# Kernel tuning notes

Hardware: AMD Instinct MI355X
Metric: run time of the kernel (lower is better)

## Reference

```python
import jax, jax.numpy as jnp
import numpy as np

B, N, F = 64, 1024, 256  # batch, graph_size, feature dim


def setup_inputs() -> dict:
    key = jax.random.key(0)
    k1, k2, k3, k4, k5 = jax.random.split(key, 5)
    x = jax.random.normal(k1, (B, F), dtype=jnp.float32)
    nodes = jax.random.normal(k2, (B, N, F), dtype=jnp.float32)
    adj = jax.random.uniform(k3, (B, N, N), dtype=jnp.float32)
    # num_nodes in [0, N]; values == N trigger the overflow/wrap path
    num_nodes = jax.random.randint(k4, (B,), 0, N + 1)
    # GNN weight for the dense GCN layer: tanh(adj @ nodes @ W)
    W = jax.random.normal(k5, (F, F), dtype=jnp.float32) * 0.05
    return {"x": x, "nodes": nodes, "adj": adj, "num_nodes": num_nodes, "W": W}


def _wrap_overflow(nodes, adj, num_nodes):
    # FIFO eviction for overflowing batches: zero slot 0 (row/col), roll up by one.
    mask = (num_nodes + 1) > N  # [B]
    w_nodes = jnp.roll(nodes.at[:, 0, :].set(0.0), shift=-1, axis=1)
    w_adj = jnp.roll(adj.at[:, 0, :].set(0.0).at[:, :, 0].set(0.0),
                     shift=(-1, -1), axis=(1, 2))
    nodes = jnp.where(mask[:, None, None], w_nodes, nodes)
    adj = jnp.where(mask[:, None, None], w_adj, adj)
    num_nodes = jnp.where(mask, num_nodes - 1, num_nodes)
    return nodes, adj, num_nodes


def reference(x, nodes, adj, num_nodes, W):
    # 1) wrap-around eviction where the graph is full (masked -> jit friendly;
    #    identical to torch branch since untouched batches are unchanged)
    nodes, adj, num_nodes = _wrap_overflow(nodes, adj, num_nodes)

    # 2) scatter-write new memory x into slot num_nodes[b] of each batch
    b_idx = jnp.arange(B)
    nodes = nodes.at[b_idx, num_nodes].set(x)

    # 3) GNN: dense GCN layer node_feats = tanh((adj @ nodes) @ W)
    node_feats = jnp.tanh(jnp.einsum('bnm,bmf->bnf', adj, nodes) @ W)

    # 4) query: read back the just-written node's embedding (pooled=False)
    mx = node_feats[b_idx, num_nodes]

    return mx, nodes, adj, num_nodes + 1
```

## Files before the change

kernel.cpp:

```cpp
#include <hip/hip_runtime.h>
#include <math.h>

#define B 64
#define N 1024
#define F 256

#define OUT_MX    0
#define OUT_NODES (B * F)
#define OUT_ADJ   (OUT_NODES + B * N * F)
#define OUT_NN    (OUT_ADJ + B * N * N)

__global__ void k_zero(float* __restrict__ t) {
    int i = blockIdx.x * 256 + threadIdx.x;
    if (i < B * F) t[i] = 0.0f;
}

__global__ void k_nodes(const float* __restrict__ x,
                        const float* __restrict__ nodes,
                        const int* __restrict__ num_nodes,
                        float* __restrict__ out) {
    int tid = threadIdx.x;
    int row_in_block = tid >> 6;
    int f4 = (tid & 63) << 2;
    long bi = (long)blockIdx.x * 4 + row_in_block;
    int b = (int)(bi >> 10);
    int i = (int)(bi & (N - 1));
    int nn_in = num_nodes[b];
    bool wrapped = (nn_in == N);
    int nn = wrapped ? (N - 1) : nn_in;
    float4 v;
    if (i == nn) {
        v = *(const float4*)(x + (long)b * F + f4);
    } else {
        long srow = wrapped ? (bi + 1) : bi;
        v = *(const float4*)(nodes + srow * F + f4);
    }
    *(float4*)(out + OUT_NODES + bi * F + f4) = v;
}

__global__ void k_adj(const float* __restrict__ adj,
                      const int* __restrict__ num_nodes,
                      float* __restrict__ out) {
    long bi = blockIdx.x;
    int b = (int)(bi >> 10);
    int i = (int)(bi & (N - 1));
    int j = threadIdx.x << 2;
    bool wrapped = (num_nodes[b] == N);
    float4 v;
    const float* base = adj + (long)b * N * N;
    if (!wrapped) {
        v = *(const float4*)(base + (long)i * N + j);
    } else if (i >= N - 1) {
        v = make_float4(0.f, 0.f, 0.f, 0.f);
    } else {
        const float* r = base + (long)(i + 1) * N;
        v.x = (j + 0 < N - 1) ? r[j + 1] : 0.f;
        v.y = (j + 1 < N - 1) ? r[j + 2] : 0.f;
        v.z = (j + 2 < N - 1) ? r[j + 3] : 0.f;
        v.w = (j + 3 < N - 1) ? r[j + 4] : 0.f;
    }
    *(float4*)(out + OUT_ADJ + bi * N + j) = v;
}

#define MCHUNK 64
__global__ void k_partial(const float* __restrict__ adj,
                          const int* __restrict__ num_nodes,
                          const float* __restrict__ out_nodes,
                          float* __restrict__ t) {
    int b = blockIdx.x >> 4;
    int s = blockIdx.x & 15;
    int nn_in = num_nodes[b];
    if (nn_in == N) return;
    int f = threadIdx.x;
    __shared__ float arow[MCHUNK];
    int m0 = s * MCHUNK;
    if (f < MCHUNK)
        arow[f] = adj[(long)b * N * N + (long)nn_in * N + m0 + f];
    __syncthreads();
    float acc = 0.0f;
    const float* np = out_nodes + ((long)b * N + m0) * F + f;
    #pragma unroll 8
    for (int m = 0; m < MCHUNK; m++)
        acc += arow[m] * np[(long)m * F];
    atomicAdd(&t[b * F + f], acc);
}

__global__ void k_final(const float* __restrict__ t,
                        const float* __restrict__ W,
                        const int* __restrict__ num_nodes,
                        float* __restrict__ out) {
    int b = blockIdx.x;
    int f = threadIdx.x;
    __shared__ float tl[F];
    tl[f] = t[b * F + f];
    __syncthreads();
    float acc = 0.0f;
    #pragma unroll 8
    for (int fp = 0; fp < F; fp++)
        acc += tl[fp] * W[fp * F + f];
    out[OUT_MX + b * F + f] = tanhf(acc);
    if (f == 0) {
        int nn_in = num_nodes[b];
        int nn = (nn_in == N) ? (N - 1) : nn_in;
        out[OUT_NN + b] = (float)(nn + 1);
    }
}

extern "C" void kernel_launch(void* const* d_in, const int* in_sizes, int n_in,
                              void* d_out, int out_size, void* d_ws, size_t ws_size,
                              hipStream_t stream) {
    const float* x         = (const float*)d_in[0];
    const float* nodes     = (const float*)d_in[1];
    const float* adj       = (const float*)d_in[2];
    const int*   num_nodes = (const int*)d_in[3];
    const float* W         = (const float*)d_in[4];
    float* out = (float*)d_out;
    float* t   = (float*)d_ws;

    hipLaunchKernelGGL(k_zero,    dim3((B * F) / 256), dim3(256), 0, stream, t);
    hipLaunchKernelGGL(k_nodes,   dim3((B * N) / 4),   dim3(256), 0, stream,
                       x, nodes, num_nodes, out);
    hipLaunchKernelGGL(k_adj,     dim3(B * N),         dim3(256), 0, stream,
                       adj, num_nodes, out);
    hipLaunchKernelGGL(k_partial, dim3(B * 16),        dim3(256), 0, stream,
                       adj, num_nodes, out + OUT_NODES, t);
    hipLaunchKernelGGL(k_final,   dim3(B),             dim3(256), 0, stream,
                       t, W, num_nodes, out);
}
```

Before: 560.1 us.

## Fuse node copy, adj copy and partial GEMV into one kernel, drop atomics

New measurement: 559.5 us. About the same (-0.1%).

```diff
diff --git a/kernel.cpp b/kernel.cpp
--- a/kernel.cpp
+++ b/kernel.cpp
@@ -10,93 +10,98 @@
 #define OUT_ADJ   (OUT_NODES + B * N * F)
 #define OUT_NN    (OUT_ADJ + B * N * N)
 
-__global__ void k_zero(float* __restrict__ t) {
-    int i = blockIdx.x * 256 + threadIdx.x;
-    if (i < B * F) t[i] = 0.0f;
+#define NODES_BLOCKS (B * 16)
+#define ADJ_BLOCKS   (B * N / 4)
+
+__global__ void k_main(const float* __restrict__ x,
+                       const float* __restrict__ nodes,
+                       const float* __restrict__ adj,
+                       const int* __restrict__ num_nodes,
+                       float* __restrict__ out,
+                       float* __restrict__ partial) {
+    __shared__ float arow[64];
+    int blk = blockIdx.x;
+    int t = threadIdx.x;
+
+    if (blk < NODES_BLOCKS) {
+        int b = blk >> 4;
+        int s = blk & 15;
+        int m0 = s << 6;
+        int nn_in = num_nodes[b];
+        bool wrapped = (nn_in == N);
+        int nn = wrapped ? (N - 1) : nn_in;
+        if (t < 64)
+            arow[t] = wrapped ? 0.0f
+                              : adj[((long)b * N + nn) * N + m0 + t];
+        __syncthreads();
+
+        int g  = t >> 6;
+        int f4 = (t & 63) << 2;
+        const float* xrow   = x + (long)b * F;
+        const float* innode = nodes + (long)b * N * F;
+        float* onode = out + OUT_NODES + ((long)b * N + m0) * F;
+        float4 acc = make_float4(0.f, 0.f, 0.f, 0.f);
+        #pragma unroll
+        for (int it = 0; it < 16; ++it) {
+            int r = (it << 2) + g;
+            int row = m0 + r;
+            float4 v;
+            if (row == nn) {
+                v = *(const float4*)(xrow + f4);
+            } else {
+                int srow = wrapped ? (row + 1) : row;
+                v = *(const float4*)(innode + (long)srow * F + f4);
+            }
+            *(float4*)(onode + (long)r * F + f4) = v;
+            float a = arow[r];
+            acc.x += a * v.x; acc.y += a * v.y;
+            acc.z += a * v.z; acc.w += a * v.w;
+        }
+        *(float4*)(partial + ((long)(b << 6) + (s << 2) + g) * F + f4) = acc;
+    } else {
+        long rb = (long)(blk - NODES_BLOCKS) << 2;
+        int j = t << 2;
+        #pragma unroll
+        for (int k = 0; k < 4; ++k) {
+            long bi = rb + k;
+            int b = (int)(bi >> 10);
+            int i = (int)(bi & (N - 1));
+            bool wrapped = (num_nodes[b] == N);
+            const float* base = adj + (long)b * N * N;
+            float4 v;
+            if (!wrapped) {
+                v = *(const float4*)(base + (long)i * N + j);
+            } else if (i >= N - 1) {
+                v = make_float4(0.f, 0.f, 0.f, 0.f);
+            } else {
+                const float* r2 = base + (long)(i + 1) * N;
+                v.x = (j + 0 < N - 1) ? r2[j + 1] : 0.f;
+                v.y = (j + 1 < N - 1) ? r2[j + 2] : 0.f;
+                v.z = (j + 2 < N - 1) ? r2[j + 3] : 0.f;
+                v.w = (j + 3 < N - 1) ? r2[j + 4] : 0.f;
+            }
+            *(float4*)(out + OUT_ADJ + bi * N + j) = v;
+        }
+    }
 }
 
-__global__ void k_nodes(const float* __restrict__ x,
-                        const float* __restrict__ nodes,
-                        const int* __restrict__ num_nodes,
-                        float* __restrict__ out) {
-    int tid = threadIdx.x;
-    int row_in_block = tid >> 6;
-    int f4 = (tid & 63) << 2;
-    long bi = (long)blockIdx.x * 4 + row_in_block;
-    int b = (int)(bi >> 10);
-    int i = (int)(bi & (N - 1));
-    int nn_in = num_nodes[b];
-    bool wrapped = (nn_in == N);
-    int nn = wrapped ? (N - 1) : nn_in;
-    float4 v;
-    if (i == nn) {
-        v = *(const float4*)(x + (long)b * F + f4);
-    } else {
-        long srow = wrapped ? (bi + 1) : bi;
-        v = *(const float4*)(nodes + srow * F + f4);
-    }
-    *(float4*)(out + OUT_NODES + bi * F + f4) = v;
-}
-
-__global__ void k_adj(const float* __restrict__ adj,
-                      const int* __restrict__ num_nodes,
-                      float* __restrict__ out) {
-    long bi = blockIdx.x;
-    int b = (int)(bi >> 10);
-    int i = (int)(bi & (N - 1));
-    int j = threadIdx.x << 2;
-    bool wrapped = (num_nodes[b] == N);
-    float4 v;
-    const float* base = adj + (long)b * N * N;
-    if (!wrapped) {
-        v = *(const float4*)(base + (long)i * N + j);
-    } else if (i >= N - 1) {
-        v = make_float4(0.f, 0.f, 0.f, 0.f);
-    } else {
-        const float* r = base + (long)(i + 1) * N;
-        v.x = (j + 0 < N - 1) ? r[j + 1] : 0.f;
-        v.y = (j + 1 < N - 1) ? r[j + 2] : 0.f;
-        v.z = (j + 2 < N - 1) ? r[j + 3] : 0.f;
-        v.w = (j + 3 < N - 1) ? r[j + 4] : 0.f;
-    }
-    *(float4*)(out + OUT_ADJ + bi * N + j) = v;
-}
-
-#define MCHUNK 64
-__global__ void k_partial(const float* __restrict__ adj,
-                          const int* __restrict__ num_nodes,
-                          const float* __restrict__ out_nodes,
-                          float* __restrict__ t) {
-    int b = blockIdx.x >> 4;
-    int s = blockIdx.x & 15;
-    int nn_in = num_nodes[b];
-    if (nn_in == N) return;
-    int f = threadIdx.x;
-    __shared__ float arow[MCHUNK];
-    int m0 = s * MCHUNK;
-    if (f < MCHUNK)
-        arow[f] = adj[(long)b * N * N + (long)nn_in * N + m0 + f];
-    __syncthreads();
-    float acc = 0.0f;
-    const float* np = out_nodes + ((long)b * N + m0) * F + f;
-    #pragma unroll 8
-    for (int m = 0; m < MCHUNK; m++)
-        acc += arow[m] * np[(long)m * F];
-    atomicAdd(&t[b * F + f], acc);
-}
-
-__global__ void k_final(const float* __restrict__ t,
+__global__ void k_final(const float* __restrict__ partial,
                         const float* __restrict__ W,
                         const int* __restrict__ num_nodes,
                         float* __restrict__ out) {
     int b = blockIdx.x;
     int f = threadIdx.x;
     __shared__ float tl[F];
-    tl[f] = t[b * F + f];
+    float s = 0.0f;
+    const float* p = partial + ((long)b << 6) * F + f;
+    #pragma unroll 8
+    for (int k = 0; k < 64; ++k)
+        s += p[(long)k * F];
+    tl[f] = s;
     __syncthreads();
     float acc = 0.0f;
     #pragma unroll 8
-    for (int fp = 0; fp < F; fp++)
+    for (int fp = 0; fp < F; ++fp)
         acc += tl[fp] * W[fp * F + f];
     out[OUT_MX + b * F + f] = tanhf(acc);
     if (f == 0) {
@@ -114,16 +119,11 @@
     const float* adj       = (const float*)d_in[2];
     const int*   num_nodes = (const int*)d_in[3];
     const float* W         = (const float*)d_in[4];
-    float* out = (float*)d_out;
-    float* t   = (float*)d_ws;
+    float* out     = (float*)d_out;
+    float* partial = (float*)d_ws;
 
-    hipLaunchKernelGGL(k_zero,    dim3((B * F) / 256), dim3(256), 0, stream, t);
-    hipLaunchKernelGGL(k_nodes,   dim3((B * N) / 4),   dim3(256), 0, stream,
-                       x, nodes, num_nodes, out);
-    hipLaunchKernelGGL(k_adj,     dim3(B * N),         dim3(256), 0, stream,
-                       adj, num_nodes, out);
-    hipLaunchKernelGGL(k_partial, dim3(B * 16),        dim3(256), 0, stream,
-                       adj, num_nodes, out + OUT_NODES, t);
-    hipLaunchKernelGGL(k_final,   dim3(B),             dim3(256), 0, stream,
-                       t, W, num_nodes, out);
+    hipLaunchKernelGGL(k_main, dim3(NODES_BLOCKS + ADJ_BLOCKS), dim3(256), 0,
+                       stream, x, nodes, adj, num_nodes, out, partial);
+    hipLaunchKernelGGL(k_final, dim3(B), dim3(256), 0, stream,
+                       partial, W, num_nodes, out);
 }
```
